# Kernel tuning notes

Measured on AMD Instinct MI355X. Metric: run time of the kernel, lower is better.

## Reference

```python
import jax, jax.numpy as jnp
import numpy as np

HIDDEN = 2048
HEADS = 16
HEAD_DIM = HIDDEN // HEADS  # 128
THETA = 10000.0


def _rope_cache(seq_len, dim, theta=THETA):
    inv_freq = 1.0 / (theta ** (jnp.arange(0, dim, 2, dtype=jnp.float32) / dim))
    t = jnp.arange(seq_len, dtype=jnp.float32)
    freqs = jnp.outer(t, inv_freq)            # [S, dim/2]
    emb = jnp.concatenate([freqs, freqs], -1)  # [S, dim]
    return jnp.cos(emb), jnp.sin(emb)


def _rotate_half(x):
    x1, x2 = jnp.split(x, 2, axis=-1)
    return jnp.concatenate([-x2, x1], axis=-1)


def setup_inputs() -> dict:
    key = jax.random.key(0)
    ks = jax.random.split(key, 5)
    B, S = 2, 2048
    scale = 1.0 / np.sqrt(HIDDEN)
    return {
        "hidden_states": jax.random.normal(ks[0], (B, S, HIDDEN), jnp.float32),
        "wq": jax.random.normal(ks[1], (HIDDEN, HIDDEN), jnp.float32) * scale,
        "wk": jax.random.normal(ks[2], (HIDDEN, HIDDEN), jnp.float32) * scale,
        "wv": jax.random.normal(ks[3], (HIDDEN, HIDDEN), jnp.float32) * scale,
        "wo": jax.random.normal(ks[4], (HIDDEN, HIDDEN), jnp.float32) * scale,
    }


def reference(hidden_states, wq, wk, wv, wo):
    B, S, D = hidden_states.shape
    H, Hd = HEADS, HEAD_DIM
    # projections (nn.Linear: x @ W^T), reshape to [B, H, S, Hd]
    def proj(w):
        return (hidden_states @ w.T).reshape(B, S, H, Hd).transpose(0, 2, 1, 3)
    q, k, v = proj(wq), proj(wk), proj(wv)
    # RoPE
    cos, sin = _rope_cache(S, Hd)             # [S, Hd]
    q = q * cos + _rotate_half(q) * sin
    k = k * cos + _rotate_half(k) * sin
    # scaled dot-product attention with causal mask
    scores = jnp.einsum("bhqd,bhkd->bhqk", q, k) / jnp.sqrt(jnp.float32(Hd))
    causal = jnp.tril(jnp.ones((S, S), bool))
    scores = jnp.where(causal, scores, -jnp.inf)
    attn = jax.nn.softmax(scores, axis=-1)
    out = jnp.einsum("bhqk,bhkd->bhqd", attn, v)  # [B, H, S, Hd]
    out = out.transpose(0, 2, 1, 3).reshape(B, S, D)
    return out @ wo.T
```

## Files before the change

kernel.cpp:

```cpp
#include <hip/hip_runtime.h>
#include <hip/hip_bf16.h>

#define S_LEN  2048
#define BATCH  2
#define NH     16
#define HD     128
#define HIDDEN 2048
#define MROWS  (BATCH*S_LEN)

typedef __attribute__((ext_vector_type(8))) short bf16x8;
typedef __attribute__((ext_vector_type(4))) short s16x4;
typedef __attribute__((ext_vector_type(4))) float f32x4;

__device__ __forceinline__ float bf2f(short s) {
    union { float f; unsigned int u; } v;
    v.u = ((unsigned int)(unsigned short)s) << 16;
    return v.f;
}
__device__ __forceinline__ short f2bf(float f) {
    union { float f; unsigned int u; } v;
    v.f = f;
    unsigned int r = v.u + 0x7fffu + ((v.u >> 16) & 1u);
    return (short)(r >> 16);
}
__device__ __forceinline__ f32x4 mfma16(bf16x8 a, bf16x8 b, f32x4 c) {
    return __builtin_amdgcn_mfma_f32_16x16x32_bf16(a, b, c, 0, 0, 0);
}
__device__ __forceinline__ void gload16(const void* g, void* l) {
    __builtin_amdgcn_global_load_lds(
        (const __attribute__((address_space(1))) void*)g,
        (__attribute__((address_space(3))) void*)l, 16, 0, 0);
}
#define SBAR()  asm volatile("s_barrier" ::: "memory")
#define LGKM0() do { asm volatile("s_waitcnt lgkmcnt(0)" ::: "memory"); \
                     __builtin_amdgcn_sched_barrier(0); } while (0)

#define SEG (4194304)
__global__ void cast_k(const float* hs, const float* wq, const float* wk,
                       const float* wv, const float* wo, short* dst)
{
    size_t i = ((size_t)blockIdx.x * 256 + threadIdx.x) * 8;
    int seg = (int)(i >> 22);
    const float* s;
    size_t off;
    if (seg < 2)      { s = hs; off = i; }
    else if (seg == 2){ s = wq; off = i - 2 * (size_t)SEG; }
    else if (seg == 3){ s = wk; off = i - 3 * (size_t)SEG; }
    else if (seg == 4){ s = wv; off = i - 4 * (size_t)SEG; }
    else              { s = wo; off = i - 5 * (size_t)SEG; }
    f32x4 lo = *(const f32x4*)(s + off);
    f32x4 hi = *(const f32x4*)(s + off + 4);
    short v[8];
#pragma unroll
    for (int j = 0; j < 4; ++j) { v[j] = f2bf(lo[j]); v[4 + j] = f2bf(hi[j]); }
    *(bf16x8*)(dst + i) = *(bf16x8*)v;
}

template<int MODE>
__global__ __launch_bounds__(512, 1)
void gemm8p(const short* A, const short* W0, const short* W1, const short* W2,
            short* Oq, short* Ok, short* Ov, float* Of)
{
    __shared__ short lds[49152];

    const int tid  = threadIdx.x;
    const int lane = tid & 63;
    const int wv   = tid >> 6;
    const int wr   = wv & 3, wc = wv >> 2;
    const int fr   = lane & 15, fg = lane >> 4;

    const int mt = blockIdx.x;
    int nt = blockIdx.y;
    const short* W = W0;
    short* Ob = Oq;
    int osel = 0;
    if (MODE == 0) {
        osel = nt >> 4; nt &= 15;
        W  = (osel == 0) ? W0 : (osel == 1) ? W1 : W2;
        Ob = (osel == 0) ? Oq : (osel == 1) ? Ok : Ov;
    }
    const int row0 = mt * 256, col0 = nt * 128;

#define STAGEH(hh)                                                              \
    do {                                                                        \
        const int sl_ = (hh) & 3;                                               \
        const int kg_ = (hh) * 32;                                              \
        _Pragma("unroll")                                                       \
        for (int it_ = 0; it_ < 2; ++it_) {                                     \
            int c_ = it_ * 512 + tid;                                           \
            int ln_ = c_ >> 3;                                                  \
            int cr_ = (c_ & 7) ^ (ln_ & 7);                                     \
            int sr_ = 2 * ln_ + (cr_ >> 2);                                     \
            int sk_ = (cr_ & 3) * 8;                                            \
            gload16(A + (size_t)(row0 + sr_) * HIDDEN + kg_ + sk_,              \
                    (char*)lds + sl_ * 16384 + c_ * 16);                        \
        }                                                                       \
        {                                                                       \
            int c_ = tid;                                                       \
            int ln_ = c_ >> 3;                                                  \
            int cr_ = (c_ & 7) ^ (ln_ & 7);                                     \
            int sr_ = 2 * ln_ + (cr_ >> 2);                                     \
            int sk_ = (cr_ & 3) * 8;                                            \
            gload16(W + (size_t)(col0 + sr_) * HIDDEN + kg_ + sk_,              \
                    (char*)lds + 65536 + sl_ * 8192 + c_ * 16);                 \
        }                                                                       \
    } while (0)

    auto ldsA = [&](int sl, int r, int kc) -> bf16x8 {
        int ln = r >> 1;
        int cs = (((r & 1) << 2) + kc) ^ (ln & 7);
        return *(const bf16x8*)((const char*)lds + sl * 16384 + ln * 128 + cs * 16);
    };
    auto ldsB = [&](int sl, int r, int kc) -> bf16x8 {
        int ln = r >> 1;
        int cs = (((r & 1) << 2) + kc) ^ (ln & 7);
        return *(const bf16x8*)((const char*)lds + 65536 + sl * 8192 + ln * 128 + cs * 16);
    };

    f32x4 acc[4][4];
#pragma unroll
    for (int m = 0; m < 4; ++m)
#pragma unroll
        for (int n = 0; n < 4; ++n) acc[m][n] = (f32x4){0.f, 0.f, 0.f, 0.f};

    STAGEH(0); STAGEH(1); STAGEH(2);
    asm volatile("s_waitcnt vmcnt(6)" ::: "memory");
    SBAR();

#pragma unroll 1
    for (int h = 0; h < 64; ++h) {
        const int sl = h & 3;
        bf16x8 b0 = ldsB(sl, wc * 64 +  0 + fr, fg);
        bf16x8 b1 = ldsB(sl, wc * 64 + 16 + fr, fg);
        bf16x8 b2 = ldsB(sl, wc * 64 + 32 + fr, fg);
        bf16x8 b3 = ldsB(sl, wc * 64 + 48 + fr, fg);
        bf16x8 a0 = ldsA(sl, wr * 64 +  0 + fr, fg);
        bf16x8 a1 = ldsA(sl, wr * 64 + 16 + fr, fg);
        if (h + 3 < 64) STAGEH(h + 3);
        SBAR();
        LGKM0();
        __builtin_amdgcn_s_setprio(1);
        acc[0][0] = mfma16(a0, b0, acc[0][0]);
        acc[0][1] = mfma16(a0, b1, acc[0][1]);
        acc[0][2] = mfma16(a0, b2, acc[0][2]);
        acc[0][3] = mfma16(a0, b3, acc[0][3]);
        acc[1][0] = mfma16(a1, b0, acc[1][0]);
        acc[1][1] = mfma16(a1, b1, acc[1][1]);
        acc[1][2] = mfma16(a1, b2, acc[1][2]);
        acc[1][3] = mfma16(a1, b3, acc[1][3]);
        __builtin_amdgcn_s_setprio(0);
        SBAR();
        bf16x8 a2 = ldsA(sl, wr * 64 + 32 + fr, fg);
        bf16x8 a3 = ldsA(sl, wr * 64 + 48 + fr, fg);
        SBAR();
        LGKM0();
        __builtin_amdgcn_s_setprio(1);
        acc[2][0] = mfma16(a2, b0, acc[2][0]);
        acc[2][1] = mfma16(a2, b1, acc[2][1]);
        acc[2][2] = mfma16(a2, b2, acc[2][2]);
        acc[2][3] = mfma16(a2, b3, acc[2][3]);
        acc[3][0] = mfma16(a3, b0, acc[3][0]);
        acc[3][1] = mfma16(a3, b1, acc[3][1]);
        acc[3][2] = mfma16(a3, b2, acc[3][2]);
        acc[3][3] = mfma16(a3, b3, acc[3][3]);
        __builtin_amdgcn_s_setprio(0);
        if (h < 61) asm volatile("s_waitcnt vmcnt(6)" ::: "memory");
        else        asm volatile("s_waitcnt vmcnt(0)" ::: "memory");
        SBAR();
    }
#undef STAGEH

    if (MODE == 0 && osel == 2) {
#pragma unroll
        for (int m = 0; m < 4; ++m)
#pragma unroll
            for (int j = 0; j < 4; ++j) {
                int row = wr * 64 + m * 16 + fg * 4 + j;
#pragma unroll
                for (int n = 0; n < 4; ++n) {
                    int col = wc * 64 + n * 16 + fr;
                    lds[col * 256 + (((row >> 3) ^ (col & 31)) * 8) + (row & 7)] =
                        f2bf(acc[m][n][j]);
                }
            }
        __syncthreads();
        const int b_ = row0 >> 11;
        const int bh = b_ * NH + nt;
        const int s0 = row0 & (S_LEN - 1);
#pragma unroll
        for (int it = 0; it < 8; ++it) {
            int c = it * 512 + tid;
            int d = c >> 5, sc = c & 31;
            bf16x8 vv = *(const bf16x8*)&lds[d * 256 + ((sc ^ (d & 31)) * 8)];
            *(bf16x8*)(Ov + ((size_t)bh * HD + d) * S_LEN + s0 + sc * 8) = vv;
        }
    } else {
#pragma unroll
        for (int m = 0; m < 4; ++m)
#pragma unroll
            for (int j = 0; j < 4; ++j) {
                int mrow = row0 + wr * 64 + m * 16 + fg * 4 + j;
#pragma unroll
                for (int n = 0; n < 4; ++n) {
                    int col = col0 + wc * 64 + n * 16 + fr;
                    float val = acc[m][n][j];
                    if (MODE == 0) {
                        int b_ = mrow >> 11, s = mrow & (S_LEN - 1);
                        int h_ = col >> 7, d = col & (HD - 1);
                        Ob[((size_t)(b_ * NH + h_) * S_LEN + s) * HD + d] = f2bf(val);
                    } else {
                        Of[(size_t)mrow * HIDDEN + col] = val;
                    }
                }
            }
    }
}

__global__ void rope_table_k(float* tab)
{
    int i = blockIdx.x * 256 + threadIdx.x;
    if (i >= S_LEN * 64) return;
    int s = i >> 6, d = i & 63;
    float inv = 1.0f / powf(10000.0f, (float)d * (1.0f / 64.0f));
    float ang = (float)s * inv;
    tab[2 * i]     = cosf(ang);
    tab[2 * i + 1] = sinf(ang);
}

__global__ void rope_apply_k(short* Q, short* K, const float* tab)
{
    int i = blockIdx.x * 256 + threadIdx.x;
    int d8 = i & 7;
    int s  = (i >> 3) & (S_LEN - 1);
    int bh = i >> 14;
    size_t base = ((size_t)bh * S_LEN + s) * HD + d8 * 8;
    const float* tp = tab + (s * 64 + d8 * 8) * 2;
    f32x4 t[4];
#pragma unroll
    for (int j = 0; j < 4; ++j) t[j] = *(const f32x4*)(tp + j * 4);

    bf16x8 q1 = *(bf16x8*)(Q + base), q2 = *(bf16x8*)(Q + base + 64);
    bf16x8 k1 = *(bf16x8*)(K + base), k2 = *(bf16x8*)(K + base + 64);
    short oq1[8], oq2[8], ok1[8], ok2[8];
    const float qs = 0.08838834764831845f;
#pragma unroll
    for (int j = 0; j < 8; ++j) {
        float c  = t[j >> 1][(j & 1) * 2];
        float sn = t[j >> 1][(j & 1) * 2 + 1];
        float a1 = bf2f(q1[j]), a2 = bf2f(q2[j]);
        oq1[j] = f2bf((a1 * c - a2 * sn) * qs);
        oq2[j] = f2bf((a2 * c + a1 * sn) * qs);
        float b1 = bf2f(k1[j]), b2 = bf2f(k2[j]);
        ok1[j] = f2bf(b1 * c - b2 * sn);
        ok2[j] = f2bf(b2 * c + b1 * sn);
    }
    *(bf16x8*)(Q + base)      = *(bf16x8*)oq1;
    *(bf16x8*)(Q + base + 64) = *(bf16x8*)oq2;
    *(bf16x8*)(K + base)      = *(bf16x8*)ok1;
    *(bf16x8*)(K + base + 64) = *(bf16x8*)ok2;
}

__global__ __launch_bounds__(256, 2)
void attn_k(const short* Q, const short* K, const short* Vt, short* AO)
{
    __shared__ short Ks[2][64 * 128];
    __shared__ short Vs[2][128 * 64];

    const int tid = threadIdx.x, lane = tid & 63, wv = tid >> 6;
    const int fr = lane & 15, fg = lane >> 4;
    const int bid = blockIdx.x;
    const int bh   = bid & 31;
    const int sub  = bid >> 5;
    const int p    = sub >> 1;
    const int half = sub & 1;

    const short* Qb = Q  + (size_t)bh * S_LEN * HD;
    const short* Kb = K  + (size_t)bh * S_LEN * HD;
    const short* Vb = Vt + (size_t)bh * HD * S_LEN;
    const int b_ = bh >> 4, h = bh & 15;

#define SWK(r) (((r) & 3) | ((((r) >> 3) & 3) << 2))
#define STAGE(t, bufi)                                                          \
    do {                                                                        \
        const int kb_ = (t) * 64;                                               \
        _Pragma("unroll")                                                       \
        for (int i_ = 0; i_ < 4; ++i_) {                                        \
            int c_ = i_ * 256 + tid;                                            \
            int r_ = c_ >> 4, bb_ = c_ & 15;                                    \
            gload16(Kb + (size_t)(kb_ + r_) * HD + ((bb_ ^ SWK(r_)) * 8),       \
                    (char*)&Ks[bufi][0] + (i_ * 256 + wv * 64) * 16);           \
        }                                                                       \
        _Pragma("unroll")                                                       \
        for (int i_ = 0; i_ < 4; ++i_) {                                        \
            int c_ = i_ * 256 + tid;                                            \
            int r_ = c_ >> 3, bb_ = c_ & 7;                                     \
            gload16(Vb + (size_t)r_ * S_LEN + kb_ + ((bb_ ^ (r_ & 7)) * 8),     \
                    (char*)&Vs[bufi][0] + (i_ * 256 + wv * 64) * 16);           \
        }                                                                       \
    } while (0)

#pragma unroll 1
    for (int phase = 0; phase < 2; ++phase) {
        const int qt = phase ? (15 - p) : p;
        const int qbase = qt * 128 + half * 64 + wv * 16;

        bf16x8 qf[4];
#pragma unroll
        for (int ks = 0; ks < 4; ++ks)
            qf[ks] = *(const bf16x8*)(Qb + (size_t)(qbase + fr) * HD
                                      + ks * 32 + fg * 8);

        f32x4 oT[8];
#pragma unroll
        for (int nd = 0; nd < 8; ++nd) oT[nd] = (f32x4){0.f, 0.f, 0.f, 0.f};
        float mrun = -1e30f, lrun = 0.f;

        const int ntiles = qt * 2 + 1 + half;
        __syncthreads();
        STAGE(0, 0);

        for (int t = 0; t < ntiles; ++t) {
            const int buf = t & 1;
            __syncthreads();
            if (t + 1 < ntiles) STAGE(t + 1, buf ^ 1);
            const int kb = t * 64;

            if (kb <= qbase + 15) {
                f32x4 sc[4];
#pragma unroll
                for (int ni = 0; ni < 4; ++ni) sc[ni] = (f32x4){0.f, 0.f, 0.f, 0.f};
                __builtin_amdgcn_s_setprio(1);
#pragma unroll
                for (int ks = 0; ks < 4; ++ks) {
                    bf16x8 kf[4];
#pragma unroll
                    for (int ni = 0; ni < 4; ++ni) {
                        int rk = ((ni & 1) << 5) + ((fr >> 2) << 3)
                               + ((ni >> 1) << 2) + (fr & 3);
                        kf[ni] = *(const bf16x8*)&Ks[buf][rk * 128
                                     + (((ks * 4 + fg) ^ fr) * 8)];
                    }
#pragma unroll
                    for (int ni = 0; ni < 4; ++ni)
                        sc[ni] = mfma16(kf[ni], qf[ks], sc[ni]);
                }
                __builtin_amdgcn_s_setprio(0);
                const int qrow = qbase + fr;
                if (kb + 63 > qbase) {
#pragma unroll
                    for (int ni = 0; ni < 4; ++ni)
#pragma unroll
                        for (int j = 0; j < 4; ++j) {
                            int kcol = kb + ((ni & 1) << 5) + (fg << 3)
                                     + ((ni >> 1) << 2) + j;
                            if (kcol > qrow) sc[ni][j] = -1e30f;
                        }
                }
                float mx = sc[0][0];
#pragma unroll
                for (int ni = 0; ni < 4; ++ni)
#pragma unroll
                    for (int j = 0; j < 4; ++j) mx = fmaxf(mx, sc[ni][j]);
                mx = fmaxf(mx, __shfl_xor(mx, 16));
                mx = fmaxf(mx, __shfl_xor(mx, 32));
                if (mx > mrun) {
                    float scale = __expf(mrun - mx);
                    mrun = mx;
                    lrun *= scale;
#pragma unroll
                    for (int nd = 0; nd < 8; ++nd)
#pragma unroll
                        for (int j = 0; j < 4; ++j) oT[nd][j] *= scale;
                }
                float rs = 0.f;
                short pw[16];
#pragma unroll
                for (int ni = 0; ni < 4; ++ni)
#pragma unroll
                    for (int j = 0; j < 4; ++j) {
                        float pe = __expf(sc[ni][j] - mrun);
                        rs += pe;
                        pw[((ni & 1) << 3) + ((ni >> 1) << 2) + j] = f2bf(pe);
                    }
                bf16x8 pf0 = *(bf16x8*)&pw[0];
                bf16x8 pf1 = *(bf16x8*)&pw[8];
                rs += __shfl_xor(rs, 16);
                rs += __shfl_xor(rs, 32);
                lrun += rs;
                __builtin_amdgcn_s_setprio(1);
#pragma unroll
                for (int nd = 0; nd < 8; ++nd) {
                    const int d = nd * 16 + fr;
                    bf16x8 vf0 = *(const bf16x8*)&Vs[buf][d * 64 + ((fg ^ (d & 7)) * 8)];
                    bf16x8 vf1 = *(const bf16x8*)&Vs[buf][d * 64 + (((4 + fg) ^ (d & 7)) * 8)];
                    oT[nd] = mfma16(vf0, pf0, oT[nd]);
                    oT[nd] = mfma16(vf1, pf1, oT[nd]);
                }
                __builtin_amdgcn_s_setprio(0);
            }
        }

        float inv = 1.0f / lrun;
        int srow = qbase + fr;
#pragma unroll
        for (int nd = 0; nd < 8; ++nd) {
            s16x4 w;
#pragma unroll
            for (int j = 0; j < 4; ++j) w[j] = f2bf(oT[nd][j] * inv);
            *(s16x4*)(AO + ((size_t)b_ * S_LEN + srow) * HIDDEN
                      + h * HD + nd * 16 + fg * 4) = w;
        }
    }
#undef STAGE
#undef SWK
}

extern "C" void kernel_launch(void* const* d_in, const int* in_sizes, int n_in,
                              void* d_out, int out_size, void* d_ws, size_t ws_size,
                              hipStream_t stream)
{
    const float* hs = (const float*)d_in[0];
    const float* wq = (const float*)d_in[1];
    const float* wk = (const float*)d_in[2];
    const float* wvp = (const float*)d_in[3];
    const float* wo = (const float*)d_in[4];
    float* out = (float*)d_out;

    char* ws = (char*)d_ws;
    short* CB  = (short*)ws;
    short* Hb  = CB;
    short* Wqb = CB + 2 * (size_t)SEG;
    short* Wkb = CB + 3 * (size_t)SEG;
    short* Wvb = CB + 4 * (size_t)SEG;
    short* Wob = CB + 5 * (size_t)SEG;
    short* Qb  = (short*)(ws + 50331648);
    short* Kb  = (short*)(ws + 67108864);
    short* Vb  = (short*)(ws + 83886080);
    short* AO  = Hb;
    float* tab = (float*)(ws + 100663296);

    cast_k<<<dim3(12288), dim3(256), 0, stream>>>(hs, wq, wk, wvp, wo, CB);
    rope_table_k<<<dim3(512), dim3(256), 0, stream>>>(tab);
    gemm8p<0><<<dim3(16, 48), dim3(512), 0, stream>>>(
        Hb, Wqb, Wkb, Wvb, Qb, Kb, Vb, nullptr);
    rope_apply_k<<<dim3(2048), dim3(256), 0, stream>>>(Qb, Kb, tab);
    attn_k<<<dim3(512), dim3(256), 0, stream>>>(Qb, Kb, Vb, AO);
    gemm8p<1><<<dim3(16, 16), dim3(512), 0, stream>>>(
        AO, Wob, nullptr, nullptr, nullptr, nullptr, nullptr, out);
}
```

Before: 366.5 us.

## Switch GEMM mainloop to K=64 tiles with triple-buffered LDS

The projection GEMM now stages 64-wide K tiles into three LDS slots instead of 32-wide K tiles into four slots, which halves the number of loop iterations and barriers per output tile. The LDS swizzle layout is simplified to one row per 128-byte line, and each iteration runs two 16-MFMA bursts with all A and B fragments loaded up front. The aim is to cut barrier and issue overhead per MFMA. In exchange it uses more LDS (144KB), holds more fragment registers, and keeps only two tiles in flight ahead of compute. A barrier is added before the epilogue reuses LDS.

```diff
diff --git a/kernel.cpp b/kernel.cpp
--- a/kernel.cpp
+++ b/kernel.cpp
@@ -61,7 +61,7 @@
 void gemm8p(const short* A, const short* W0, const short* W1, const short* W2,
             short* Oq, short* Ok, short* Ov, float* Of)
 {
-    __shared__ short lds[49152];
+    __shared__ short lds[73728];
 
     const int tid  = threadIdx.x;
     const int lane = tid & 63;
@@ -81,40 +81,34 @@
     }
     const int row0 = mt * 256, col0 = nt * 128;
 
-#define STAGEH(hh)                                                              \
+#define STAGET(t_, sl_)                                                         \
     do {                                                                        \
-        const int sl_ = (hh) & 3;                                               \
-        const int kg_ = (hh) * 32;                                              \
+        const int kg_ = (t_) * 64;                                              \
+        _Pragma("unroll")                                                       \
+        for (int it_ = 0; it_ < 4; ++it_) {                                     \
+            int c_ = it_ * 512 + tid;                                           \
+            int r_ = c_ >> 3;                                                   \
+            gload16(A + (size_t)(row0 + r_) * HIDDEN + kg_                      \
+                        + (((c_ & 7) ^ (r_ & 7)) * 8),                          \
+                    (char*)lds + (sl_) * 49152 + c_ * 16);                      \
+        }                                                                       \
         _Pragma("unroll")                                                       \
         for (int it_ = 0; it_ < 2; ++it_) {                                     \
             int c_ = it_ * 512 + tid;                                           \
-            int ln_ = c_ >> 3;                                                  \
-            int cr_ = (c_ & 7) ^ (ln_ & 7);                                     \
-            int sr_ = 2 * ln_ + (cr_ >> 2);                                     \
-            int sk_ = (cr_ & 3) * 8;                                            \
-            gload16(A + (size_t)(row0 + sr_) * HIDDEN + kg_ + sk_,              \
-                    (char*)lds + sl_ * 16384 + c_ * 16);                        \
-        }                                                                       \
-        {                                                                       \
-            int c_ = tid;                                                       \
-            int ln_ = c_ >> 3;                                                  \
-            int cr_ = (c_ & 7) ^ (ln_ & 7);                                     \
-            int sr_ = 2 * ln_ + (cr_ >> 2);                                     \
-            int sk_ = (cr_ & 3) * 8;                                            \
-            gload16(W + (size_t)(col0 + sr_) * HIDDEN + kg_ + sk_,              \
-                    (char*)lds + 65536 + sl_ * 8192 + c_ * 16);                 \
+            int r_ = c_ >> 3;                                                   \
+            gload16(W + (size_t)(col0 + r_) * HIDDEN + kg_                      \
+                        + (((c_ & 7) ^ (r_ & 7)) * 8),                          \
+                    (char*)lds + (sl_) * 49152 + 32768 + c_ * 16);              \
         }                                                                       \
     } while (0)
 
     auto ldsA = [&](int sl, int r, int kc) -> bf16x8 {
-        int ln = r >> 1;
-        int cs = (((r & 1) << 2) + kc) ^ (ln & 7);
-        return *(const bf16x8*)((const char*)lds + sl * 16384 + ln * 128 + cs * 16);
+        return *(const bf16x8*)((const char*)lds + sl * 49152
+                                + r * 128 + ((kc ^ (r & 7)) * 16));
     };
     auto ldsB = [&](int sl, int r, int kc) -> bf16x8 {
-        int ln = r >> 1;
-        int cs = (((r & 1) << 2) + kc) ^ (ln & 7);
-        return *(const bf16x8*)((const char*)lds + 65536 + sl * 8192 + ln * 128 + cs * 16);
+        return *(const bf16x8*)((const char*)lds + sl * 49152 + 32768
+                                + r * 128 + ((kc ^ (r & 7)) * 16));
     };
 
     f32x4 acc[4][4];
@@ -123,20 +117,24 @@
 #pragma unroll
         for (int n = 0; n < 4; ++n) acc[m][n] = (f32x4){0.f, 0.f, 0.f, 0.f};
 
-    STAGEH(0); STAGEH(1); STAGEH(2);
+    const int NT = HIDDEN / 64;
+    STAGET(0, 0);
+    STAGET(1, 1);
     asm volatile("s_waitcnt vmcnt(6)" ::: "memory");
     SBAR();
 
 #pragma unroll 1
-    for (int h = 0; h < 64; ++h) {
-        const int sl = h & 3;
+    for (int t = 0; t < NT; ++t) {
+        const int sl = t % 3;
+        bf16x8 a0 = ldsA(sl, wr * 64 +  0 + fr, fg);
+        bf16x8 a1 = ldsA(sl, wr * 64 + 16 + fr, fg);
+        bf16x8 a2 = ldsA(sl, wr * 64 + 32 + fr, fg);
+        bf16x8 a3 = ldsA(sl, wr * 64 + 48 + fr, fg);
         bf16x8 b0 = ldsB(sl, wc * 64 +  0 + fr, fg);
         bf16x8 b1 = ldsB(sl, wc * 64 + 16 + fr, fg);
         bf16x8 b2 = ldsB(sl, wc * 64 + 32 + fr, fg);
         bf16x8 b3 = ldsB(sl, wc * 64 + 48 + fr, fg);
-        bf16x8 a0 = ldsA(sl, wr * 64 +  0 + fr, fg);
-        bf16x8 a1 = ldsA(sl, wr * 64 + 16 + fr, fg);
-        if (h + 3 < 64) STAGEH(h + 3);
+        if (t + 2 < NT) STAGET(t + 2, (t + 2) % 3);
         SBAR();
         LGKM0();
         __builtin_amdgcn_s_setprio(1);
@@ -148,13 +146,6 @@
         acc[1][1] = mfma16(a1, b1, acc[1][1]);
         acc[1][2] = mfma16(a1, b2, acc[1][2]);
         acc[1][3] = mfma16(a1, b3, acc[1][3]);
-        __builtin_amdgcn_s_setprio(0);
-        SBAR();
-        bf16x8 a2 = ldsA(sl, wr * 64 + 32 + fr, fg);
-        bf16x8 a3 = ldsA(sl, wr * 64 + 48 + fr, fg);
-        SBAR();
-        LGKM0();
-        __builtin_amdgcn_s_setprio(1);
         acc[2][0] = mfma16(a2, b0, acc[2][0]);
         acc[2][1] = mfma16(a2, b1, acc[2][1]);
         acc[2][2] = mfma16(a2, b2, acc[2][2]);
@@ -164,13 +155,43 @@
         acc[3][2] = mfma16(a3, b2, acc[3][2]);
         acc[3][3] = mfma16(a3, b3, acc[3][3]);
         __builtin_amdgcn_s_setprio(0);
-        if (h < 61) asm volatile("s_waitcnt vmcnt(6)" ::: "memory");
-        else        asm volatile("s_waitcnt vmcnt(0)" ::: "memory");
+        SBAR();
+        a0 = ldsA(sl, wr * 64 +  0 + fr, 4 + fg);
+        a1 = ldsA(sl, wr * 64 + 16 + fr, 4 + fg);
+        a2 = ldsA(sl, wr * 64 + 32 + fr, 4 + fg);
+        a3 = ldsA(sl, wr * 64 + 48 + fr, 4 + fg);
+        b0 = ldsB(sl, wc * 64 +  0 + fr, 4 + fg);
+        b1 = ldsB(sl, wc * 64 + 16 + fr, 4 + fg);
+        b2 = ldsB(sl, wc * 64 + 32 + fr, 4 + fg);
+        b3 = ldsB(sl, wc * 64 + 48 + fr, 4 + fg);
+        SBAR();
+        LGKM0();
+        __builtin_amdgcn_s_setprio(1);
+        acc[0][0] = mfma16(a0, b0, acc[0][0]);
+        acc[0][1] = mfma16(a0, b1, acc[0][1]);
+        acc[0][2] = mfma16(a0, b2, acc[0][2]);
+        acc[0][3] = mfma16(a0, b3, acc[0][3]);
+        acc[1][0] = mfma16(a1, b0, acc[1][0]);
+        acc[1][1] = mfma16(a1, b1, acc[1][1]);
+        acc[1][2] = mfma16(a1, b2, acc[1][2]);
+        acc[1][3] = mfma16(a1, b3, acc[1][3]);
+        acc[2][0] = mfma16(a2, b0, acc[2][0]);
+        acc[2][1] = mfma16(a2, b1, acc[2][1]);
+        acc[2][2] = mfma16(a2, b2, acc[2][2]);
+        acc[2][3] = mfma16(a2, b3, acc[2][3]);
+        acc[3][0] = mfma16(a3, b0, acc[3][0]);
+        acc[3][1] = mfma16(a3, b1, acc[3][1]);
+        acc[3][2] = mfma16(a3, b2, acc[3][2]);
+        acc[3][3] = mfma16(a3, b3, acc[3][3]);
+        __builtin_amdgcn_s_setprio(0);
+        if (t + 2 < NT) asm volatile("s_waitcnt vmcnt(6)" ::: "memory");
+        else            asm volatile("s_waitcnt vmcnt(0)" ::: "memory");
         SBAR();
     }
-#undef STAGEH
+#undef STAGET
 
     if (MODE == 0 && osel == 2) {
+        __syncthreads();
 #pragma unroll
         for (int m = 0; m < 4; ++m)
 #pragma unroll
```

Result: faster. 359.3 us (-2.0%).
